# Kernel tuning notes

Measured on AMD Instinct MI355X. Metric: run time of the kernel, lower is better.

## Reference

```python
import jax, jax.numpy as jnp
import numpy as np

TOP_K = 8
N_GROUP = 8
TOPK_GROUP = 4
ROUTED_SCALE = 2.5


def setup_inputs() -> dict:
    key = jax.random.key(0)
    ks = jax.random.split(key, 7)
    T, H, E, I, SI = 4096, 1024, 32, 512, 2048
    W = 0.05  # weight scale to keep relu^2 activations sane
    return {
        "hidden_states": jax.random.normal(ks[0], (T, H), jnp.float32),
        "gate_w": jax.random.normal(ks[1], (E, H), jnp.float32) * W,
        "bias": jax.random.normal(ks[2], (E,), jnp.float32),
        "w_up": jax.random.normal(ks[3], (E, I, H), jnp.float32) * W,
        "w_down": jax.random.normal(ks[4], (E, H, I), jnp.float32) * W,
        "shared_up": jax.random.normal(ks[5], (SI, H), jnp.float32) * W,
        "shared_down": jax.random.normal(ks[6], (H, SI), jnp.float32) * W,
    }


def _grouped_topk_sigmoid(logits, bias):
    # vLLM grouped_topk with scoring_func='sigmoid' + e_score_correction_bias
    T, E = logits.shape
    scores = jax.nn.sigmoid(logits)                       # [T, E]
    sfc = scores + bias[None, :]                          # scores for choice
    g = sfc.reshape(T, N_GROUP, E // N_GROUP)
    group_scores = jnp.sum(jax.lax.top_k(g, 2)[0], -1)    # [T, G] sum of top-2
    grp_idx = jax.lax.top_k(group_scores, TOPK_GROUP)[1]  # [T, topk_group]
    gmask = jnp.zeros((T, N_GROUP), bool).at[jnp.arange(T)[:, None], grp_idx].set(True)
    emask = jnp.repeat(gmask, E // N_GROUP, axis=1)       # [T, E]
    masked = jnp.where(emask, sfc, -jnp.inf)
    topk_ids = jax.lax.top_k(masked, TOP_K)[1]            # [T, K]
    topk_w = jnp.take_along_axis(scores, topk_ids, axis=1)  # weights from raw scores
    topk_w = topk_w / jnp.sum(topk_w, axis=-1, keepdims=True)  # renormalize
    return topk_w, topk_ids


def reference(hidden_states, gate_w, bias, w_up, w_down, shared_up, shared_down):
    x = hidden_states
    T, H = x.shape
    E = gate_w.shape[0]
    # router (fp32 gate)
    logits = x.astype(jnp.float32) @ gate_w.T
    topk_w, topk_ids = _grouped_topk_sigmoid(logits, bias)
    # dense combine weights [T, E] (zero for unselected experts)
    gates = jnp.zeros((T, E), x.dtype).at[jnp.arange(T)[:, None], topk_ids].set(
        topk_w.astype(x.dtype))
    # routed experts: relu^2 MLP (no gating mul), combined with gate weights
    h = jnp.einsum('th,eih->tei', x, w_up)                # [T, E, I]
    h = jnp.square(jax.nn.relu(h))
    routed = jnp.einsum('tei,te,ehi->th', h, gates, w_down)
    # shared expert (same relu^2 MLP)
    s = jnp.square(jax.nn.relu(x @ shared_up.T)) @ shared_down.T
    return routed * ROUTED_SCALE + s
```

## Files before the change

kernel.cpp:

```cpp
#include <hip/hip_runtime.h>
#include <hip/hip_bf16.h>


typedef _Float16 h8 __attribute__((ext_vector_type(8)));
typedef _Float16 h4 __attribute__((ext_vector_type(4)));
typedef float f4 __attribute__((ext_vector_type(4)));

#define T_TOK 4096
#define HDIM  1024
#define NEXP  32
#define IDIM  512
#define SIDIM 2048
#define TOPK  8
#define MAXTU 224
#define MAXTD 160

__device__ __forceinline__ int xcd_swz(int orig, int n) {
    int q = n >> 3, r = n & 7;
    int x = orig & 7, idx = orig >> 3;
    return (x < r ? x * (q + 1) : r * (q + 1) + (x - r) * q) + idx;
}

__device__ __forceinline__ void gload16(const void* g, void* l) {
    __builtin_amdgcn_global_load_lds(
        (const __attribute__((address_space(1))) void*)g,
        (__attribute__((address_space(3))) void*)l, 16, 0, 0);
}

__global__ __launch_bounds__(256) void cvt_all_kernel(
    const float* __restrict__ sA, _Float16* __restrict__ dA, int nA,
    const float* __restrict__ sB, _Float16* __restrict__ dB, int nB,
    const float* __restrict__ sC, _Float16* __restrict__ dC, int nC,
    const float* __restrict__ sD, _Float16* __restrict__ dD, int nD,
    const float* __restrict__ sE, _Float16* __restrict__ dE, int nE) {
    const int total = nA + nB + nC + nD + nE;
    for (int gi = blockIdx.x * 256 + threadIdx.x; gi < total; gi += gridDim.x * 256) {
        const float* s; _Float16* d; int i = gi;
        if (i < nA) { s = sA; d = dA; }
        else { i -= nA;
        if (i < nB) { s = sB; d = dB; }
        else { i -= nB;
        if (i < nC) { s = sC; d = dC; }
        else { i -= nC;
        if (i < nD) { s = sD; d = dD; }
        else { i -= nD; s = sE; d = dE; } } } }
        float4 v = reinterpret_cast<const float4*>(s)[i];
        h4 h; h[0] = (_Float16)v.x; h[1] = (_Float16)v.y; h[2] = (_Float16)v.z; h[3] = (_Float16)v.w;
        reinterpret_cast<h4*>(d)[i] = h;
    }
}

__global__ __launch_bounds__(256) void logits_select_kernel(
    const float* __restrict__ x, const float* __restrict__ gw,
    const float* __restrict__ bias, int* __restrict__ topk_ids,
    float* __restrict__ topk_w) {
    const int t0  = blockIdx.x * 16;
    const int tid = threadIdx.x;
    __shared__ double xS[16][66];
    __shared__ double gS[32][65];
    __shared__ double sS[16][33];
    __shared__ double sfcS[16][33];
    const int e  = tid & 31;
    const int tg = tid >> 5;
    const int tA = tg * 2, tB = tg * 2 + 1;
    double acc0 = 0.0, acc1 = 0.0;

    for (int kc = 0; kc < HDIM; kc += 64) {
        {
            int r = tid >> 4, c0 = (tid & 15) * 4;
            float4 v = *reinterpret_cast<const float4*>(x + (size_t)(t0 + r) * HDIM + kc + c0);
            xS[r][c0]     = (double)v.x;
            xS[r][c0 + 1] = (double)v.y;
            xS[r][c0 + 2] = (double)v.z;
            xS[r][c0 + 3] = (double)v.w;
        }
        {
            int r = tid >> 3, c0 = (tid & 7) * 8;
            const float* gp = gw + (size_t)r * HDIM + kc + c0;
            float4 v0 = *reinterpret_cast<const float4*>(gp);
            float4 v1 = *reinterpret_cast<const float4*>(gp + 4);
            gS[r][c0]     = (double)v0.x;
            gS[r][c0 + 1] = (double)v0.y;
            gS[r][c0 + 2] = (double)v0.z;
            gS[r][c0 + 3] = (double)v0.w;
            gS[r][c0 + 4] = (double)v1.x;
            gS[r][c0 + 5] = (double)v1.y;
            gS[r][c0 + 6] = (double)v1.z;
            gS[r][c0 + 7] = (double)v1.w;
        }
        __syncthreads();
#pragma unroll
        for (int k = 0; k < 64; ++k) {
            double g = gS[e][k];
            acc0 = fma(g, xS[tA][k], acc0);
            acc1 = fma(g, xS[tB][k], acc1);
        }
        __syncthreads();
    }
    {
        double s0 = 1.0 / (1.0 + exp(-acc0));
        double s1 = 1.0 / (1.0 + exp(-acc1));
        double b = (double)bias[e];
        sS[tA][e] = s0;  sfcS[tA][e] = s0 + b;
        sS[tB][e] = s1;  sfcS[tB][e] = s1 + b;
    }
    __syncthreads();

    if (tid < 16) {
        const int t = t0 + tid;
        double gsc[8];
        for (int g = 0; g < 8; ++g) {
            double m1 = -1e300, m2 = -1e300;
            for (int j = 0; j < 4; ++j) {
                double v = sfcS[tid][g * 4 + j];
                if (v > m1) { m2 = m1; m1 = v; } else if (v > m2) { m2 = v; }
            }
            gsc[g] = m1 + m2;
        }
        bool gsel[8] = {};
        for (int r = 0; r < 4; ++r) {
            int best = 0; double bv = -1e300;
            for (int g = 0; g < 8; ++g)
                if (!gsel[g] && gsc[g] > bv) { bv = gsc[g]; best = g; }
            gsel[best] = true;
        }
        bool esel[32];
        for (int i2 = 0; i2 < 32; ++i2) esel[i2] = false;
        int ids[8]; double wsum = 0.0;
        for (int r = 0; r < 8; ++r) {
            int best = 0; double bv = -1e300;
            for (int e2 = 0; e2 < 32; ++e2)
                if (gsel[e2 >> 2] && !esel[e2] && sfcS[tid][e2] > bv) { bv = sfcS[tid][e2]; best = e2; }
            esel[best] = true;
            ids[r] = best;
            wsum += sS[tid][best];
        }
        for (int r = 0; r < 8; ++r) {
            topk_ids[t * TOPK + r] = ids[r];
            topk_w[t * TOPK + r] = (float)(sS[tid][ids[r]] / wsum * 2.5);
        }
    }
}

__global__ void build_scan_kernel(const int* __restrict__ ids, const float* __restrict__ w,
                                  int* __restrict__ tok_list, float* __restrict__ wt_list,
                                  int* __restrict__ dest_list, int* __restrict__ counts,
                                  int* __restrict__ offsets, int* __restrict__ tmapU,
                                  int* __restrict__ tmapD, int* __restrict__ done) {
    const int e = blockIdx.x;
    const int lane = threadIdx.x;
    int base = 0;
    for (int t0 = 0; t0 < T_TOK; t0 += 64) {
        int t = t0 + lane;
        int found = -1;
#pragma unroll
        for (int k = 0; k < TOPK; ++k)
            if (ids[t * TOPK + k] == e) found = k;
        unsigned long long mask = __ballot(found >= 0);
        if (found >= 0) {
            int pos = base + __popcll(mask & ((1ull << lane) - 1ull));
            tok_list[e * T_TOK + pos]  = t;
            wt_list[e * T_TOK + pos]   = w[t * TOPK + found];
            dest_list[e * T_TOK + pos] = t * TOPK + found;
        }
        base += __popcll(mask);
    }
    if (lane == 0) counts[e] = base;
    __threadfence();
    if (lane == 0 && atomicAdd(done, 1) == NEXP - 1) {
        int run = 0, ntu = 0, ntd = 0;
        for (int ee = 0; ee < NEXP; ++ee) {
            offsets[ee] = run;
            int c = counts[ee];
            for (int m0 = 0; m0 < c; m0 += 256) {
                tmapU[1 + 2 * ntu] = ee; tmapU[2 + 2 * ntu] = m0; ++ntu;
                tmapD[1 + 2 * ntd] = ee; tmapD[2 + 2 * ntd] = m0; ++ntd;
            }
            run += c;
        }
        offsets[NEXP] = run;
        for (int c = 0; c < 4; ++c)
            for (int m0 = 0; m0 < T_TOK; m0 += 256) {
                tmapU[1 + 2 * ntu] = NEXP + c; tmapU[2 + 2 * ntu] = m0; ++ntu;
            }
        tmapU[0] = ntu;
        tmapD[0] = ntd;
    }
}

__device__ __forceinline__ void gemm8p(const _Float16* const (&aP)[4],
                                       const _Float16* const (&bP)[4],
                                       const int nt, f4 (&acc)[8][4]) {
    __shared__ __attribute__((aligned(16))) _Float16 As[2][256 * 64];
    __shared__ __attribute__((aligned(16))) _Float16 Bs[2][256 * 64];
    const int tid = threadIdx.x;
    const int w = tid >> 6, lane = tid & 63;
    const int wr = w >> 2, wc = w & 3;
    const int ra = lane & 15, kq = lane >> 4;
    const int ldsb = w * 512;
    const int arow = wr * 128 + ra;
    const int brow = wc * 64 + ra;
    const int ch0 = (kq ^ (ra & 7)) << 3;
    const int ch1 = ((4 + kq) ^ (ra & 7)) << 3;

#pragma unroll
    for (int j = 0; j < 4; ++j) gload16(aP[j], &As[0][j * 4096 + ldsb]);
#pragma unroll
    for (int j = 0; j < 4; ++j) gload16(bP[j], &Bs[0][j * 4096 + ldsb]);

    for (int t = 0; t < nt; ++t) {
        const int buf = t & 1, nb = buf ^ 1;
        const bool pf = (t + 1 < nt);
        const int ko = (t + 1) * 64;

        asm volatile("s_waitcnt vmcnt(0)" ::: "memory");
        __builtin_amdgcn_s_barrier();
        asm volatile("" ::: "memory");

        h8 bf0[4], af0[4];
#pragma unroll
        for (int n = 0; n < 4; ++n)
            bf0[n] = *reinterpret_cast<const h8*>(&Bs[buf][(brow + n * 16) * 64 + ch0]);
#pragma unroll
        for (int m = 0; m < 4; ++m)
            af0[m] = *reinterpret_cast<const h8*>(&As[buf][(arow + m * 16) * 64 + ch0]);
        if (pf) {
            gload16(aP[0] + ko, &As[nb][0 * 4096 + ldsb]);
            gload16(aP[1] + ko, &As[nb][1 * 4096 + ldsb]);
        }
        h8 af1[4];
#pragma unroll
        for (int m = 0; m < 4; ++m)
            af1[m] = *reinterpret_cast<const h8*>(&As[buf][(arow + (m + 4) * 16) * 64 + ch0]);
        if (pf) {
            gload16(aP[2] + ko, &As[nb][2 * 4096 + ldsb]);
            gload16(aP[3] + ko, &As[nb][3 * 4096 + ldsb]);
        }
        __builtin_amdgcn_s_setprio(1);
#pragma unroll
        for (int m = 0; m < 4; ++m)
#pragma unroll
            for (int n = 0; n < 4; ++n)
                acc[m][n] = __builtin_amdgcn_mfma_f32_16x16x32_f16(af0[m], bf0[n], acc[m][n], 0, 0, 0);
        __builtin_amdgcn_s_setprio(0);
        if (pf) {
            gload16(bP[0] + ko, &Bs[nb][0 * 4096 + ldsb]);
            gload16(bP[1] + ko, &Bs[nb][1 * 4096 + ldsb]);
        }
        h8 bf1[4], af2[4];
#pragma unroll
        for (int n = 0; n < 4; ++n)
            bf1[n] = *reinterpret_cast<const h8*>(&Bs[buf][(brow + n * 16) * 64 + ch1]);
#pragma unroll
        for (int m = 0; m < 4; ++m)
            af2[m] = *reinterpret_cast<const h8*>(&As[buf][(arow + m * 16) * 64 + ch1]);
        __builtin_amdgcn_s_setprio(1);
#pragma unroll
        for (int m = 0; m < 4; ++m)
#pragma unroll
            for (int n = 0; n < 4; ++n)
                acc[m + 4][n] = __builtin_amdgcn_mfma_f32_16x16x32_f16(af1[m], bf0[n], acc[m + 4][n], 0, 0, 0);
        __builtin_amdgcn_s_setprio(0);
        if (pf) {
            gload16(bP[2] + ko, &Bs[nb][2 * 4096 + ldsb]);
            gload16(bP[3] + ko, &Bs[nb][3 * 4096 + ldsb]);
        }
        h8 af3[4];
#pragma unroll
        for (int m = 0; m < 4; ++m)
            af3[m] = *reinterpret_cast<const h8*>(&As[buf][(arow + (m + 4) * 16) * 64 + ch1]);
        __builtin_amdgcn_s_setprio(1);
#pragma unroll
        for (int m = 0; m < 4; ++m)
#pragma unroll
            for (int n = 0; n < 4; ++n)
                acc[m][n] = __builtin_amdgcn_mfma_f32_16x16x32_f16(af2[m], bf1[n], acc[m][n], 0, 0, 0);
#pragma unroll
        for (int m = 0; m < 4; ++m)
#pragma unroll
            for (int n = 0; n < 4; ++n)
                acc[m + 4][n] = __builtin_amdgcn_mfma_f32_16x16x32_f16(af3[m], bf1[n], acc[m + 4][n], 0, 0, 0);
        __builtin_amdgcn_s_setprio(0);

        asm volatile("" ::: "memory");
        __builtin_amdgcn_s_barrier();
        asm volatile("" ::: "memory");
    }
}

__global__ __launch_bounds__(512, 2) void up_kernel(
    const _Float16* __restrict__ xh, const _Float16* __restrict__ whup,
    const _Float16* __restrict__ shupW,
    const int* __restrict__ tok_list, const float* __restrict__ wt_list,
    const int* __restrict__ counts, const int* __restrict__ offsets,
    const int* __restrict__ tmap,
    _Float16* __restrict__ hbuf, _Float16* __restrict__ shb) {
    const int ntile = tmap[0];
    int ti = blockIdx.x;
    if (ti >= ntile) return;
    ti = xcd_swz(ti, ntile);
    const int e  = tmap[1 + 2 * ti];
    const int m0 = tmap[2 + 2 * ti];
    const int n0 = blockIdx.y * 256;
    const bool routed = e < NEXP;
    const int cnt = routed ? counts[e] : T_TOK;

    __shared__ int   tokS[256];
    __shared__ float wS[256];
    const int tid = threadIdx.x;
    if (tid < 256) {
        int row = m0 + tid;
        int cr = row < cnt ? row : cnt - 1;
        if (routed) {
            tokS[tid] = tok_list[e * T_TOK + cr];
            wS[tid]   = row < cnt ? wt_list[e * T_TOK + row] : 0.f;
        } else {
            tokS[tid] = cr;
            wS[tid]   = 1.f;
        }
    }
    __syncthreads();

    const int w = tid >> 6, lane = tid & 63;
    const int swz = ((lane & 7) ^ (lane >> 3)) << 3;
    const int rr = w * 8 + (lane >> 3);
    const _Float16* bbase = routed ? (whup + (size_t)e * IDIM * HDIM)
                                   : (shupW + (size_t)(e - NEXP) * 512 * HDIM);
    const _Float16* aP[4]; const _Float16* bP[4];
#pragma unroll
    for (int j = 0; j < 4; ++j) {
        aP[j] = xh + (size_t)tokS[j * 64 + rr] * HDIM + swz;
        bP[j] = bbase + (size_t)(n0 + j * 64 + rr) * HDIM + swz;
    }
    f4 acc[8][4] = {};
    gemm8p(aP, bP, HDIM / 64, acc);

    const int wr = w >> 2, wc = w & 3;
    const int kq = lane >> 4, ra = lane & 15;
    _Float16* obase; size_t ostr;
    if (routed) { obase = hbuf + (size_t)(offsets[e] + m0) * IDIM + n0; ostr = IDIM; }
    else        { obase = shb + (size_t)m0 * SIDIM + (size_t)(e - NEXP) * 512 + n0; ostr = SIDIM; }
#pragma unroll
    for (int m = 0; m < 8; ++m)
#pragma unroll
    for (int r = 0; r < 4; ++r) {
        int orow = wr * 128 + m * 16 + kq * 4 + r;
        if (m0 + orow < cnt) {
            float g = wS[orow];
#pragma unroll
            for (int n = 0; n < 4; ++n) {
                float v = fmaxf(acc[m][n][r], 0.f);
                obase[(size_t)orow * ostr + wc * 64 + n * 16 + ra] = (_Float16)(v * v * g);
            }
        }
    }
}

template<bool SLOT>
__global__ __launch_bounds__(512, 2) void down_routed_kernel(
    const _Float16* __restrict__ hbuf, const _Float16* __restrict__ whdown,
    const int* __restrict__ dest_list, const int* __restrict__ counts,
    const int* __restrict__ offsets, const int* __restrict__ tmap,
    _Float16* __restrict__ slotout, float* __restrict__ out) {
    const int ntile = tmap[0];
    int ti = blockIdx.x;
    if (ti >= ntile) return;
    ti = xcd_swz(ti, ntile);
    const int e   = tmap[1 + 2 * ti];
    const int m0  = tmap[2 + 2 * ti];
    const int cnt = counts[e];
    const int n0   = blockIdx.y * 256;
    const int eoff = offsets[e];

    __shared__ int dS[256];
    const int tid = threadIdx.x;
    if (tid < 256) {
        int row = m0 + tid;
        dS[tid] = dest_list[e * T_TOK + (row < cnt ? row : cnt - 1)];
    }
    __syncthreads();

    const int w = tid >> 6, lane = tid & 63;
    const int swz = ((lane & 7) ^ (lane >> 3)) << 3;
    const int rr = w * 8 + (lane >> 3);
    const _Float16* aP[4]; const _Float16* bP[4];
#pragma unroll
    for (int j = 0; j < 4; ++j) {
        int row = m0 + j * 64 + rr;
        int cr  = row < cnt ? row : cnt - 1;
        aP[j] = hbuf + (size_t)(eoff + cr) * IDIM + swz;
        bP[j] = whdown + ((size_t)e * HDIM + n0 + j * 64 + rr) * IDIM + swz;
    }
    f4 acc[8][4] = {};
    gemm8p(aP, bP, IDIM / 64, acc);

    const int wr = w >> 2, wc = w & 3;
    const int kq = lane >> 4, ra = lane & 15;
#pragma unroll
    for (int m = 0; m < 8; ++m)
#pragma unroll
    for (int r = 0; r < 4; ++r) {
        int orow = wr * 128 + m * 16 + kq * 4 + r;
        if (m0 + orow < cnt) {
            int d = dS[orow];
            if (SLOT) {
                size_t rb = (size_t)d * HDIM + n0;
#pragma unroll
                for (int n = 0; n < 4; ++n)
                    slotout[rb + wc * 64 + n * 16 + ra] = (_Float16)acc[m][n][r];
            } else {
                size_t rb = (size_t)(d >> 3) * HDIM + n0;
#pragma unroll
                for (int n = 0; n < 4; ++n)
                    atomicAdd(&out[rb + wc * 64 + n * 16 + ra], acc[m][n][r]);
            }
        }
    }
}

template<int K>
__device__ __forceinline__ void gemm128(const _Float16* const (&aSrc)[4],
                                        const _Float16* const (&bSrc)[4],
                                        f4 (&acc)[4][4]) {
    __shared__ __attribute__((aligned(16))) _Float16 As[128 * 64];
    __shared__ __attribute__((aligned(16))) _Float16 Bs[128 * 64];
    const int tid  = threadIdx.x;
    const int w    = tid >> 6, lane = tid & 63;
    const int wm   = (w & 1) * 64, wn = (w >> 1) * 64;
    const int ra   = lane & 15, kq = lane >> 4;

    for (int kk = 0; kk < K; kk += 64) {
#pragma unroll
        for (int i = 0; i < 4; ++i) {
            gload16(aSrc[i] + kk, As + (size_t)(i * 256 + w * 64) * 8);
            gload16(bSrc[i] + kk, Bs + (size_t)(i * 256 + w * 64) * 8);
        }
        __syncthreads();
#pragma unroll
        for (int s = 0; s < 2; ++s) {
            h8 af[4], bf[4];
#pragma unroll
            for (int m = 0; m < 4; ++m) {
                int row = wm + m * 16 + ra;
                af[m] = *reinterpret_cast<const h8*>(As + row * 64 + (((s * 4 + kq) ^ (row & 7)) << 3));
            }
#pragma unroll
            for (int n = 0; n < 4; ++n) {
                int row = wn + n * 16 + ra;
                bf[n] = *reinterpret_cast<const h8*>(Bs + row * 64 + (((s * 4 + kq) ^ (row & 7)) << 3));
            }
#pragma unroll
            for (int m = 0; m < 4; ++m)
#pragma unroll
                for (int n = 0; n < 4; ++n)
                    acc[m][n] = __builtin_amdgcn_mfma_f32_16x16x32_f16(af[m], bf[n], acc[m][n], 0, 0, 0);
        }
        __syncthreads();
    }
}

template<bool COMB>
__global__ __launch_bounds__(256) void down_shared_kernel(
    const _Float16* __restrict__ sh, const _Float16* __restrict__ shdown,
    const _Float16* __restrict__ slotout, float* __restrict__ out) {
    const int m0 = blockIdx.y * 128;
    const int n0 = blockIdx.x * 128;
    const int tid = threadIdx.x;
    const int sc = ((tid & 7) ^ ((tid >> 3) & 7)) << 3;
    const int r0 = tid >> 3;
    const _Float16* aSrc[4]; const _Float16* bSrc[4];
#pragma unroll
    for (int i = 0; i < 4; ++i) {
        aSrc[i] = sh + (size_t)(m0 + i * 32 + r0) * SIDIM + sc;
        bSrc[i] = shdown + (size_t)(n0 + i * 32 + r0) * SIDIM + sc;
    }
    f4 acc[4][4] = {};
    gemm128<SIDIM>(aSrc, bSrc, acc);

    const int w = tid >> 6, lane = tid & 63;
    const int wm = (w & 1) * 64, wn = (w >> 1) * 64;
    const int cq = lane >> 4, cc = lane & 15;
#pragma unroll
    for (int m = 0; m < 4; ++m)
#pragma unroll
    for (int r = 0; r < 4; ++r) {
        int orow = wm + m * 16 + cq * 4 + r;
        size_t trow = (size_t)(m0 + orow);
#pragma unroll
        for (int n = 0; n < 4; ++n) {
            int col = n0 + wn + n * 16 + cc;
            float v = acc[m][n][r];
            if (COMB) {
                const _Float16* sp = slotout + trow * TOPK * HDIM + col;
#pragma unroll
                for (int k = 0; k < TOPK; ++k)
                    v += (float)sp[(size_t)k * HDIM];
            }
            out[trow * HDIM + col] = v;
        }
    }
}

extern "C" void kernel_launch(void* const* d_in, const int* in_sizes, int n_in,
                              void* d_out, int out_size, void* d_ws, size_t ws_size,
                              hipStream_t stream) {
    const float* x     = (const float*)d_in[0];
    const float* gw    = (const float*)d_in[1];
    const float* bias  = (const float*)d_in[2];
    const float* wup   = (const float*)d_in[3];
    const float* wdown = (const float*)d_in[4];
    const float* sup   = (const float*)d_in[5];
    const float* sdown = (const float*)d_in[6];
    float* out = (float*)d_out;

    char* ws = (char*)d_ws;
    size_t off = 0;
    auto take = [&](size_t bytes) {
        char* p = ws + off;
        off = (off + bytes + 255) & ~(size_t)255;
        return p;
    };
    _Float16* xh      = (_Float16*)take((size_t)T_TOK * HDIM * 2);
    _Float16* whup    = (_Float16*)take((size_t)NEXP * IDIM * HDIM * 2);
    _Float16* whdown  = (_Float16*)take((size_t)NEXP * HDIM * IDIM * 2);
    _Float16* shupW   = (_Float16*)take((size_t)SIDIM * HDIM * 2);
    _Float16* shdownW = (_Float16*)take((size_t)HDIM * SIDIM * 2);
    _Float16* sh      = (_Float16*)take((size_t)T_TOK * SIDIM * 2);
    _Float16* hbuf    = (_Float16*)take((size_t)T_TOK * TOPK * IDIM * 2);
    int*   ids       = (int*)take((size_t)T_TOK * TOPK * 4);
    float* tw        = (float*)take((size_t)T_TOK * TOPK * 4);
    int*   tok_list  = (int*)take((size_t)NEXP * T_TOK * 4);
    float* wt_list   = (float*)take((size_t)NEXP * T_TOK * 4);
    int*   dest_list = (int*)take((size_t)NEXP * T_TOK * 4);
    int*   counts    = (int*)take(NEXP * 4);
    int*   offsets   = (int*)take((NEXP + 1) * 4);
    int*   tmapU     = (int*)take((1 + 2 * MAXTU) * 4);
    int*   tmapD     = (int*)take((1 + 2 * MAXTD) * 4);
    int*   done      = (int*)take(4);
    _Float16* slotout = (_Float16*)take((size_t)T_TOK * TOPK * HDIM * 2);
    const bool use_slot = off <= ws_size;

    hipMemsetAsync(done, 0, 4, stream);

    logits_select_kernel<<<T_TOK / 16, 256, 0, stream>>>(x, gw, bias, ids, tw);
    build_scan_kernel<<<NEXP, 64, 0, stream>>>(
        ids, tw, tok_list, wt_list, dest_list, counts, offsets, tmapU, tmapD, done);

    cvt_all_kernel<<<2048, 256, 0, stream>>>(
        x, xh, T_TOK * HDIM / 4,
        wup, whup, NEXP * IDIM * HDIM / 4,
        wdown, whdown, NEXP * HDIM * IDIM / 4,
        sup, shupW, SIDIM * HDIM / 4,
        sdown, shdownW, HDIM * SIDIM / 4);

    up_kernel<<<dim3(MAXTU, 2), 512, 0, stream>>>(
        xh, whup, shupW, tok_list, wt_list, counts, offsets, tmapU, hbuf, sh);

    if (use_slot) {
        down_routed_kernel<true><<<dim3(MAXTD, HDIM / 256), 512, 0, stream>>>(
            hbuf, whdown, dest_list, counts, offsets, tmapD, slotout, out);
        down_shared_kernel<true><<<dim3(HDIM / 128, T_TOK / 128), 256, 0, stream>>>(
            sh, shdownW, slotout, out);
    } else {
        down_shared_kernel<false><<<dim3(HDIM / 128, T_TOK / 128), 256, 0, stream>>>(
            sh, shdownW, slotout, out);
        down_routed_kernel<false><<<dim3(MAXTD, HDIM / 256), 512, 0, stream>>>(
            hbuf, whdown, dest_list, counts, offsets, tmapD, slotout, out);
    }
}
```

Before: 323.0 us.

## Shrink expert GEMM tiles to 256x128 with 4-wave blocks, single-buffered LDS

Result: faster. 306.6 us, median of 3 (-5.1%).

```diff
diff --git a/kernel.cpp b/kernel.cpp
--- a/kernel.cpp
+++ b/kernel.cpp
@@ -188,107 +188,94 @@
     }
 }
 
-__device__ __forceinline__ void gemm8p(const _Float16* const (&aP)[4],
+__device__ __forceinline__ void gemm2p(const _Float16* const (&aP)[8],
                                        const _Float16* const (&bP)[4],
                                        const int nt, f4 (&acc)[8][4]) {
-    __shared__ __attribute__((aligned(16))) _Float16 As[2][256 * 64];
-    __shared__ __attribute__((aligned(16))) _Float16 Bs[2][256 * 64];
+    __shared__ __attribute__((aligned(16))) _Float16 As[256 * 64];
+    __shared__ __attribute__((aligned(16))) _Float16 Bs[128 * 64];
     const int tid = threadIdx.x;
     const int w = tid >> 6, lane = tid & 63;
-    const int wr = w >> 2, wc = w & 3;
+    const int wr = w >> 1, wc = w & 1;
     const int ra = lane & 15, kq = lane >> 4;
-    const int ldsb = w * 512;
+    const int ldsw = w * 512;
     const int arow = wr * 128 + ra;
     const int brow = wc * 64 + ra;
     const int ch0 = (kq ^ (ra & 7)) << 3;
     const int ch1 = ((4 + kq) ^ (ra & 7)) << 3;
 
-#pragma unroll
-    for (int j = 0; j < 4; ++j) gload16(aP[j], &As[0][j * 4096 + ldsb]);
-#pragma unroll
-    for (int j = 0; j < 4; ++j) gload16(bP[j], &Bs[0][j * 4096 + ldsb]);
-
     for (int t = 0; t < nt; ++t) {
-        const int buf = t & 1, nb = buf ^ 1;
-        const bool pf = (t + 1 < nt);
-        const int ko = (t + 1) * 64;
-
-        asm volatile("s_waitcnt vmcnt(0)" ::: "memory");
-        __builtin_amdgcn_s_barrier();
-        asm volatile("" ::: "memory");
-
-        h8 bf0[4], af0[4];
-#pragma unroll
-        for (int n = 0; n < 4; ++n)
-            bf0[n] = *reinterpret_cast<const h8*>(&Bs[buf][(brow + n * 16) * 64 + ch0]);
-#pragma unroll
-        for (int m = 0; m < 4; ++m)
-            af0[m] = *reinterpret_cast<const h8*>(&As[buf][(arow + m * 16) * 64 + ch0]);
-        if (pf) {
-            gload16(aP[0] + ko, &As[nb][0 * 4096 + ldsb]);
-            gload16(aP[1] + ko, &As[nb][1 * 4096 + ldsb]);
-        }
-        h8 af1[4];
-#pragma unroll
-        for (int m = 0; m < 4; ++m)
-            af1[m] = *reinterpret_cast<const h8*>(&As[buf][(arow + (m + 4) * 16) * 64 + ch0]);
-        if (pf) {
-            gload16(aP[2] + ko, &As[nb][2 * 4096 + ldsb]);
-            gload16(aP[3] + ko, &As[nb][3 * 4096 + ldsb]);
-        }
-        __builtin_amdgcn_s_setprio(1);
-#pragma unroll
-        for (int m = 0; m < 4; ++m)
-#pragma unroll
-            for (int n = 0; n < 4; ++n)
-                acc[m][n] = __builtin_amdgcn_mfma_f32_16x16x32_f16(af0[m], bf0[n], acc[m][n], 0, 0, 0);
-        __builtin_amdgcn_s_setprio(0);
-        if (pf) {
-            gload16(bP[0] + ko, &Bs[nb][0 * 4096 + ldsb]);
-            gload16(bP[1] + ko, &Bs[nb][1 * 4096 + ldsb]);
-        }
-        h8 bf1[4], af2[4];
-#pragma unroll
-        for (int n = 0; n < 4; ++n)
-            bf1[n] = *reinterpret_cast<const h8*>(&Bs[buf][(brow + n * 16) * 64 + ch1]);
-#pragma unroll
-        for (int m = 0; m < 4; ++m)
-            af2[m] = *reinterpret_cast<const h8*>(&As[buf][(arow + m * 16) * 64 + ch1]);
-        __builtin_amdgcn_s_setprio(1);
-#pragma unroll
-        for (int m = 0; m < 4; ++m)
-#pragma unroll
-            for (int n = 0; n < 4; ++n)
-                acc[m + 4][n] = __builtin_amdgcn_mfma_f32_16x16x32_f16(af1[m], bf0[n], acc[m + 4][n], 0, 0, 0);
-        __builtin_amdgcn_s_setprio(0);
-        if (pf) {
-            gload16(bP[2] + ko, &Bs[nb][2 * 4096 + ldsb]);
-            gload16(bP[3] + ko, &Bs[nb][3 * 4096 + ldsb]);
-        }
-        h8 af3[4];
-#pragma unroll
-        for (int m = 0; m < 4; ++m)
-            af3[m] = *reinterpret_cast<const h8*>(&As[buf][(arow + (m + 4) * 16) * 64 + ch1]);
-        __builtin_amdgcn_s_setprio(1);
-#pragma unroll
-        for (int m = 0; m < 4; ++m)
-#pragma unroll
-            for (int n = 0; n < 4; ++n)
-                acc[m][n] = __builtin_amdgcn_mfma_f32_16x16x32_f16(af2[m], bf1[n], acc[m][n], 0, 0, 0);
-#pragma unroll
-        for (int m = 0; m < 4; ++m)
-#pragma unroll
-            for (int n = 0; n < 4; ++n)
-                acc[m + 4][n] = __builtin_amdgcn_mfma_f32_16x16x32_f16(af3[m], bf1[n], acc[m + 4][n], 0, 0, 0);
-        __builtin_amdgcn_s_setprio(0);
-
-        asm volatile("" ::: "memory");
-        __builtin_amdgcn_s_barrier();
-        asm volatile("" ::: "memory");
-    }
-}
-
-__global__ __launch_bounds__(512, 2) void up_kernel(
+        const int ko = t * 64;
+#pragma unroll
+        for (int s = 0; s < 8; ++s)
+            gload16(aP[s] + ko, &As[s * 2048 + ldsw]);
+#pragma unroll
+        for (int s = 0; s < 4; ++s)
+            gload16(bP[s] + ko, &Bs[s * 2048 + ldsw]);
+        __syncthreads();
+
+        h8 bf0[4], bf1[4];
+#pragma unroll
+        for (int n = 0; n < 4; ++n) {
+            bf0[n] = *reinterpret_cast<const h8*>(&Bs[(brow + n * 16) * 64 + ch0]);
+            bf1[n] = *reinterpret_cast<const h8*>(&Bs[(brow + n * 16) * 64 + ch1]);
+        }
+        {
+            h8 af[4];
+#pragma unroll
+            for (int m = 0; m < 4; ++m)
+                af[m] = *reinterpret_cast<const h8*>(&As[(arow + m * 16) * 64 + ch0]);
+            __builtin_amdgcn_s_setprio(1);
+#pragma unroll
+            for (int m = 0; m < 4; ++m)
+#pragma unroll
+                for (int n = 0; n < 4; ++n)
+                    acc[m][n] = __builtin_amdgcn_mfma_f32_16x16x32_f16(af[m], bf0[n], acc[m][n], 0, 0, 0);
+            __builtin_amdgcn_s_setprio(0);
+        }
+        {
+            h8 af[4];
+#pragma unroll
+            for (int m = 0; m < 4; ++m)
+                af[m] = *reinterpret_cast<const h8*>(&As[(arow + (m + 4) * 16) * 64 + ch0]);
+            __builtin_amdgcn_s_setprio(1);
+#pragma unroll
+            for (int m = 0; m < 4; ++m)
+#pragma unroll
+                for (int n = 0; n < 4; ++n)
+                    acc[m + 4][n] = __builtin_amdgcn_mfma_f32_16x16x32_f16(af[m], bf0[n], acc[m + 4][n], 0, 0, 0);
+            __builtin_amdgcn_s_setprio(0);
+        }
+        {
+            h8 af[4];
+#pragma unroll
+            for (int m = 0; m < 4; ++m)
+                af[m] = *reinterpret_cast<const h8*>(&As[(arow + m * 16) * 64 + ch1]);
+            __builtin_amdgcn_s_setprio(1);
+#pragma unroll
+            for (int m = 0; m < 4; ++m)
+#pragma unroll
+                for (int n = 0; n < 4; ++n)
+                    acc[m][n] = __builtin_amdgcn_mfma_f32_16x16x32_f16(af[m], bf1[n], acc[m][n], 0, 0, 0);
+            __builtin_amdgcn_s_setprio(0);
+        }
+        {
+            h8 af[4];
+#pragma unroll
+            for (int m = 0; m < 4; ++m)
+                af[m] = *reinterpret_cast<const h8*>(&As[(arow + (m + 4) * 16) * 64 + ch1]);
+            __builtin_amdgcn_s_setprio(1);
+#pragma unroll
+            for (int m = 0; m < 4; ++m)
+#pragma unroll
+                for (int n = 0; n < 4; ++n)
+                    acc[m + 4][n] = __builtin_amdgcn_mfma_f32_16x16x32_f16(af[m], bf1[n], acc[m + 4][n], 0, 0, 0);
+            __builtin_amdgcn_s_setprio(0);
+        }
+        __syncthreads();
+    }
+}
+
+__global__ __launch_bounds__(256, 2) void up_kernel(
     const _Float16* __restrict__ xh, const _Float16* __restrict__ whup,
     const _Float16* __restrict__ shupW,
     const int* __restrict__ tok_list, const float* __restrict__ wt_list,
@@ -301,14 +288,14 @@
     ti = xcd_swz(ti, ntile);
     const int e  = tmap[1 + 2 * ti];
     const int m0 = tmap[2 + 2 * ti];
-    const int n0 = blockIdx.y * 256;
+    const int n0 = blockIdx.y * 128;
     const bool routed = e < NEXP;
     const int cnt = routed ? counts[e] : T_TOK;
 
     __shared__ int   tokS[256];
     __shared__ float wS[256];
     const int tid = threadIdx.x;
-    if (tid < 256) {
+    {
         int row = m0 + tid;
         int cr = row < cnt ? row : cnt - 1;
         if (routed) {
@@ -326,16 +313,18 @@
     const int rr = w * 8 + (lane >> 3);
     const _Float16* bbase = routed ? (whup + (size_t)e * IDIM * HDIM)
                                    : (shupW + (size_t)(e - NEXP) * 512 * HDIM);
-    const _Float16* aP[4]; const _Float16* bP[4];
-#pragma unroll
-    for (int j = 0; j < 4; ++j) {
-        aP[j] = xh + (size_t)tokS[j * 64 + rr] * HDIM + swz;
-        bP[j] = bbase + (size_t)(n0 + j * 64 + rr) * HDIM + swz;
-    }
+    const _Float16* aP[8]; const _Float16* bP[4];
+#pragma unroll
+    for (int s = 0; s < 8; ++s)
+        aP[s] = xh + (size_t)tokS[s * 32 + rr] * HDIM + swz;
+#pragma unroll
+    for (int s = 0; s < 4; ++s)
+        bP[s] = bbase + (size_t)(n0 + s * 32 + rr) * HDIM + swz;
+
     f4 acc[8][4] = {};
-    gemm8p(aP, bP, HDIM / 64, acc);
-
-    const int wr = w >> 2, wc = w & 3;
+    gemm2p(aP, bP, HDIM / 64, acc);
+
+    const int wr = w >> 1, wc = w & 1;
     const int kq = lane >> 4, ra = lane & 15;
     _Float16* obase; size_t ostr;
     if (routed) { obase = hbuf + (size_t)(offsets[e] + m0) * IDIM + n0; ostr = IDIM; }
@@ -357,7 +346,7 @@
 }
 
 template<bool SLOT>
-__global__ __launch_bounds__(512, 2) void down_routed_kernel(
+__global__ __launch_bounds__(256, 2) void down_routed_kernel(
     const _Float16* __restrict__ hbuf, const _Float16* __restrict__ whdown,
     const int* __restrict__ dest_list, const int* __restrict__ counts,
     const int* __restrict__ offsets, const int* __restrict__ tmap,
@@ -369,12 +358,12 @@
     const int e   = tmap[1 + 2 * ti];
     const int m0  = tmap[2 + 2 * ti];
     const int cnt = counts[e];
-    const int n0   = blockIdx.y * 256;
+    const int n0   = blockIdx.y * 128;
     const int eoff = offsets[e];
 
     __shared__ int dS[256];
     const int tid = threadIdx.x;
-    if (tid < 256) {
+    {
         int row = m0 + tid;
         dS[tid] = dest_list[e * T_TOK + (row < cnt ? row : cnt - 1)];
     }
@@ -383,18 +372,21 @@
     const int w = tid >> 6, lane = tid & 63;
     const int swz = ((lane & 7) ^ (lane >> 3)) << 3;
     const int rr = w * 8 + (lane >> 3);
-    const _Float16* aP[4]; const _Float16* bP[4];
-#pragma unroll
-    for (int j = 0; j < 4; ++j) {
-        int row = m0 + j * 64 + rr;
+    const _Float16* aP[8]; const _Float16* bP[4];
+#pragma unroll
+    for (int s = 0; s < 8; ++s) {
+        int row = m0 + s * 32 + rr;
         int cr  = row < cnt ? row : cnt - 1;
-        aP[j] = hbuf + (size_t)(eoff + cr) * IDIM + swz;
-        bP[j] = whdown + ((size_t)e * HDIM + n0 + j * 64 + rr) * IDIM + swz;
-    }
+        aP[s] = hbuf + (size_t)(eoff + cr) * IDIM + swz;
+    }
+#pragma unroll
+    for (int s = 0; s < 4; ++s)
+        bP[s] = whdown + ((size_t)e * HDIM + n0 + s * 32 + rr) * IDIM + swz;
+
     f4 acc[8][4] = {};
-    gemm8p(aP, bP, IDIM / 64, acc);
-
-    const int wr = w >> 2, wc = w & 3;
+    gemm2p(aP, bP, IDIM / 64, acc);
+
+    const int wr = w >> 1, wc = w & 1;
     const int kq = lane >> 4, ra = lane & 15;
 #pragma unroll
     for (int m = 0; m < 8; ++m)
@@ -553,18 +545,18 @@
         sup, shupW, SIDIM * HDIM / 4,
         sdown, shdownW, HDIM * SIDIM / 4);
 
-    up_kernel<<<dim3(MAXTU, 2), 512, 0, stream>>>(
+    up_kernel<<<dim3(MAXTU, 4), 256, 0, stream>>>(
         xh, whup, shupW, tok_list, wt_list, counts, offsets, tmapU, hbuf, sh);
 
     if (use_slot) {
-        down_routed_kernel<true><<<dim3(MAXTD, HDIM / 256), 512, 0, stream>>>(
+        down_routed_kernel<true><<<dim3(MAXTD, HDIM / 128), 256, 0, stream>>>(
             hbuf, whdown, dest_list, counts, offsets, tmapD, slotout, out);
         down_shared_kernel<true><<<dim3(HDIM / 128, T_TOK / 128), 256, 0, stream>>>(
             sh, shdownW, slotout, out);
     } else {
         down_shared_kernel<false><<<dim3(HDIM / 128, T_TOK / 128), 256, 0, stream>>>(
             sh, shdownW, slotout, out);
-        down_routed_kernel<false><<<dim3(MAXTD, HDIM / 256), 512, 0, stream>>>(
+        down_routed_kernel<false><<<dim3(MAXTD, HDIM / 128), 256, 0, stream>>>(
             hbuf, whdown, dest_list, counts, offsets, tmapD, slotout, out);
     }
 }
```
